# Kernel tuning notes

Hardware: AMD Instinct MI355X
Metric: run time of the kernel (lower is better)

## Reference

```python
import jax, jax.numpy as jnp
import numpy as np

B = 2097152   # ODE-state batch
DIM = 2
HM = 8        # metric hidden
HP = 8        # potential hidden
NV = 2        # number of potential nets
NLV = 1       # hidden layers per potential net


def setup_inputs() -> dict:
    key = jax.random.key(0)
    ks = jax.random.split(key, 16)
    n = lambda k, shp: jax.random.normal(k, shp, dtype=jnp.float32)
    s = 0.5  # weight scale, roughly matching default Linear init magnitude
    return {
        "t": jnp.zeros((1,), jnp.float32),
        "x": n(ks[0], (B, DIM)),
        "mW0": n(ks[1], (HM, DIM)) * s,
        "mb0": n(ks[2], (HM,)) * s,
        "mW1": n(ks[3], (HM, HM)) * s,
        "mb1": n(ks[4], (HM,)) * s,
        "mW2": n(ks[5], (4, HM)) * s,
        "mb2": n(ks[6], (4,)) * s,
        "pW1": n(ks[7], (NV, HP, DIM)) * s,
        "pb1": n(ks[8], (NV, HP)) * s,
        "pW2": n(ks[9], (NV, NLV, HP, HP)) * s,
        "pb2": n(ks[10], (NV, NLV, HP)) * s,
        "pW3": n(ks[11], (NV, 1, HP)) * s,
        "pb3": n(ks[12], (NV, 1)) * s,
    }


def reference(t, x, mW0, mb0, mW1, mb1, mW2, mb2, pW1, pb1, pW2, pb2, pW3, pb3):
    # ---- metric net: Linear->ELU chain, last layer linear, dim -> 4 ----
    h = jax.nn.elu(x @ mW0.T + mb0)
    h = jax.nn.elu(h @ mW1.T + mb1)
    bmat = h @ mW2.T + mb2                      # [B, 4]
    b1, b2, b3, b4 = (bmat[:, 0:1], bmat[:, 1:2], bmat[:, 2:3], bmat[:, 3:4])
    m2 = b1 * b2 + b3 * b4
    mag = jnp.concatenate([b1 ** 2 + b3 ** 2, m2, m2, b2 ** 2 + b4 ** 2], axis=1)  # [B, 4]

    # ---- potential nets, all n_V stacked on leading axis v ----
    f1 = jnp.tanh(jnp.einsum('bi,voi->vbo', x, pW1) + pb1[:, None, :])  # [V, B, HP]
    f2s = []
    f = f1
    for j in range(NLV):  # fixed small loop over structurally distinct layers
        f = jnp.tanh(jnp.einsum('vbp,vqp->vbq', f, pW2[:, j]) + pb2[:, j][:, None, :])
        f2s.append(f)
    f3 = jax.nn.sigmoid(jnp.einsum('vbp,vop->vbo', f, pW3) + pb3[:, None, :])  # [V, B, 1]

    # ---- hand-rolled gradient of potentials (faithful: sigmoid applied to f3 again, as in source) ----
    s = jax.nn.sigmoid(f3)
    grad = (s * (1.0 - s)) * pW3                # [V,B,1]*[V,1,HP] -> [V,B,HP]
    for j in reversed(range(NLV)):
        grad = jnp.einsum('vbq,vqp->vbp', grad * (1.0 - f2s[j] ** 2), pW2[:, j])
    grad = jnp.einsum('vbp,vpi->vbi', grad * (1.0 - f1 ** 2), pW1)  # [V, B, DIM]
    g = jnp.mean(grad, axis=0)                  # sum over n_V then / n_V  -> [B, DIM]

    # ---- combine: out = metric * repeated gradient, row-block sums ----
    g4 = jnp.tile(g, (1, 2))                    # [B, 4]
    out4 = mag * g4
    out = jnp.concatenate([out4[:, :2].sum(1, keepdims=True),
                           out4[:, 2:].sum(1, keepdims=True)], axis=1)  # [B, 2]
    return out
```

## Files before the change

### kernel.cpp

```cpp
#include <hip/hip_runtime.h>

#define NB 2097152
#define HM 8
#define HP 8
#define NV 2

typedef float v2 __attribute__((ext_vector_type(2)));

static __device__ __forceinline__ v2 splat(float s) { return (v2){s, s}; }
static __device__ __forceinline__ v2 vfma(v2 a, v2 b, v2 c) {
    return __builtin_elementwise_fma(a, b, c);
}
static __device__ __forceinline__ v2 vexp2(v2 x) {
    return (v2){__builtin_amdgcn_exp2f(x.x), __builtin_amdgcn_exp2f(x.y)};
}
static __device__ __forceinline__ v2 vclamp9(v2 x) {
    return (v2){__builtin_amdgcn_fmed3f(x.x, -9.f, 9.f),
                __builtin_amdgcn_fmed3f(x.y, -9.f, 9.f)};
}

static __device__ __forceinline__ void tanh8(const v2* z, v2* out) {
    const float a1 = 4.89352455891786e-03f, a3 = 6.37261928875436e-04f,
                a5 = 1.48572235717979e-05f, a7 = 5.12229709037114e-08f,
                a9 = -8.60467152213735e-11f, a11 = 2.00018790482477e-13f,
                a13 = -2.76076847742355e-16f;
    const float b0 = 4.89352518554385e-03f, b2 = 2.26843463243900e-03f,
                b4 = 1.18534705686654e-04f, b6 = 1.19825839466702e-06f;
    v2 p[8], q[8];
#pragma unroll
    for (int i = 0; i < 8; ++i) {
        v2 xc = vclamp9(z[i]);
        v2 t  = xc * xc;
        v2 pp = vfma(t, splat(a13), splat(a11));
        pp = vfma(t, pp, splat(a9));
        pp = vfma(t, pp, splat(a7));
        pp = vfma(t, pp, splat(a5));
        pp = vfma(t, pp, splat(a3));
        pp = vfma(t, pp, splat(a1));
        p[i] = pp * xc;
        v2 qq = vfma(t, splat(b6), splat(b4));
        qq = vfma(t, qq, splat(b2));
        q[i] = vfma(t, qq, splat(b0));
    }
#pragma unroll
    for (int g = 0; g < 2; ++g) {
        const v2* qg = q + g * 4;
        const v2* pg = p + g * 4;
        v2* og = out + g * 4;
        v2 ab = qg[0] * qg[1];
        v2 cd = qg[2] * qg[3];
        v2 abcd = ab * cd;
        v2 inv = (v2){__builtin_amdgcn_rcpf(abcd.x), __builtin_amdgcn_rcpf(abcd.y)};
        v2 s  = cd * inv;
        v2 tt = ab * inv;
        og[0] = pg[0] * (qg[1] * s);
        og[1] = pg[1] * (qg[0] * s);
        og[2] = pg[2] * (qg[3] * tt);
        og[3] = pg[3] * (qg[2] * tt);
    }
}

static __device__ __forceinline__ void elu8(const v2* z, v2* out) {
    const float L2E = 1.4426950408889634f;
#pragma unroll
    for (int i = 0; i < 8; ++i) {
        v2 e  = vexp2(z[i] * splat(L2E));
        v2 em = e - splat(1.f);
        v2 mn = __builtin_elementwise_min(em, splat(0.f));
        out[i] = __builtin_elementwise_max(z[i], mn);
    }
}

static __device__ __forceinline__ v2 vsigmoid(v2 z) {
    const float NL2E = -1.4426950408889634f;
    v2 e = vexp2(z * splat(NL2E));
    e = __builtin_elementwise_min(e, splat(1e18f));
    v2 d = e + splat(1.f);
    float pr  = d.x * d.y;
    float inv = __builtin_amdgcn_rcpf(pr);
    return (v2){inv * d.y, inv * d.x};
}

__global__ __launch_bounds__(256) void odefunc_kernel(
    const float* __restrict__ x,
    const float* __restrict__ mW0, const float* __restrict__ mb0,
    const float* __restrict__ mW1, const float* __restrict__ mb1,
    const float* __restrict__ mW2, const float* __restrict__ mb2,
    const float* __restrict__ pW1, const float* __restrict__ pb1,
    const float* __restrict__ pW2, const float* __restrict__ pb2,
    const float* __restrict__ pW3, const float* __restrict__ pb3,
    float* __restrict__ out)
{
    const int tid = blockIdx.x * blockDim.x + threadIdx.x;
    const int b0  = tid * 2;

    const float4 xv = *reinterpret_cast<const float4*>(x + b0 * 2);
    const v2 x0 = (v2){xv.x, xv.z};
    const v2 x1 = (v2){xv.y, xv.w};
    const v2 one = splat(1.f);

    v2 z[HM], h[HM], h2[HM];
#pragma unroll
    for (int o = 0; o < HM; ++o)
        z[o] = vfma(splat(mW0[o * 2]), x0,
                    vfma(splat(mW0[o * 2 + 1]), x1, splat(mb0[o])));
    elu8(z, h);
#pragma unroll
    for (int o = 0; o < HM; ++o) {
        v2 acc = splat(mb1[o]);
#pragma unroll
        for (int i = 0; i < HM; ++i) acc = vfma(splat(mW1[o * HM + i]), h[i], acc);
        z[o] = acc;
    }
    elu8(z, h2);

    v2 bm[4];
#pragma unroll
    for (int o = 0; o < 4; ++o) {
        v2 acc = splat(mb2[o]);
#pragma unroll
        for (int i = 0; i < HM; ++i) acc = vfma(splat(mW2[o * HM + i]), h2[i], acc);
        bm[o] = acc;
    }
    const v2 m2   = bm[0] * bm[1] + bm[2] * bm[3];
    const v2 mag0 = bm[0] * bm[0] + bm[2] * bm[2];
    const v2 mag3 = bm[1] * bm[1] + bm[3] * bm[3];

    v2 g0 = splat(0.f), g1 = splat(0.f);
#pragma unroll
    for (int v = 0; v < NV; ++v) {
        const float* W1 = pW1 + v * HP * 2;
        const float* B1 = pb1 + v * HP;
        const float* W2 = pW2 + v * HP * HP;
        const float* B2 = pb2 + v * HP;
        const float* W3 = pW3 + v * HP;
        const float  B3 = pb3[v];

        v2 zf[HP], f1[HP], f2[HP];
#pragma unroll
        for (int o = 0; o < HP; ++o)
            zf[o] = vfma(splat(W1[o * 2]), x0,
                         vfma(splat(W1[o * 2 + 1]), x1, splat(B1[o])));
        tanh8(zf, f1);

#pragma unroll
        for (int q = 0; q < HP; ++q) {
            v2 acc = splat(B2[q]);
#pragma unroll
            for (int p = 0; p < HP; ++p) acc = vfma(splat(W2[q * HP + p]), f1[p], acc);
            zf[q] = acc;
        }
        tanh8(zf, f2);

        v2 acc3 = splat(B3);
#pragma unroll
        for (int p = 0; p < HP; ++p) acc3 = vfma(splat(W3[p]), f2[p], acc3);
        const v2 f3 = vsigmoid(acc3);
        const v2 s  = vsigmoid(f3);
        const v2 ss = s * (one - s);

        v2 gq[HP];
#pragma unroll
        for (int q = 0; q < HP; ++q)
            gq[q] = splat(W3[q]) * vfma(-f2[q], f2[q], one);

        v2 gp[HP];
#pragma unroll
        for (int p = 0; p < HP; ++p) {
            v2 acc = splat(0.f);
#pragma unroll
            for (int q = 0; q < HP; ++q) acc = vfma(gq[q], splat(W2[q * HP + p]), acc);
            gp[p] = acc * vfma(-f1[p], f1[p], one);
        }

        v2 gi0 = splat(0.f), gi1 = splat(0.f);
#pragma unroll
        for (int p = 0; p < HP; ++p) {
            gi0 = vfma(gp[p], splat(W1[p * 2]), gi0);
            gi1 = vfma(gp[p], splat(W1[p * 2 + 1]), gi1);
        }
        g0 = vfma(ss, gi0, g0);
        g1 = vfma(ss, gi1, g1);
    }
    g0 = g0 * splat(0.5f);
    g1 = g1 * splat(0.5f);

    const v2 r0 = mag0 * g0 + m2 * g1;
    const v2 r1 = m2 * g0 + mag3 * g1;

    *reinterpret_cast<float4*>(out + b0 * 2) = make_float4(r0.x, r1.x, r0.y, r1.y);
}

extern "C" void kernel_launch(void* const* d_in, const int* in_sizes, int n_in,
                              void* d_out, int out_size, void* d_ws, size_t ws_size,
                              hipStream_t stream) {
    const float* x   = (const float*)d_in[1];
    const float* mW0 = (const float*)d_in[2];
    const float* mb0 = (const float*)d_in[3];
    const float* mW1 = (const float*)d_in[4];
    const float* mb1 = (const float*)d_in[5];
    const float* mW2 = (const float*)d_in[6];
    const float* mb2 = (const float*)d_in[7];
    const float* pW1 = (const float*)d_in[8];
    const float* pb1 = (const float*)d_in[9];
    const float* pW2 = (const float*)d_in[10];
    const float* pb2 = (const float*)d_in[11];
    const float* pW3 = (const float*)d_in[12];
    const float* pb3 = (const float*)d_in[13];
    float* out = (float*)d_out;

    const int threads = 256;
    const int blocks  = NB / (threads * 2);
    odefunc_kernel<<<blocks, threads, 0, stream>>>(
        x, mW0, mb0, mW1, mb1, mW2, mb2, pW1, pb1, pW2, pb2, pW3, pb3, out);
}
```

Measured before the change: 145.4 us.

## Replace rational tanh with exp2-based form and process four rows per thread

The rational polynomial tanh approximation is replaced by tanh = 1 - 2/(exp(2z)+1). It uses one hardware exp2 per element and keeps the shared batched-reciprocal trick, which cuts FMA count in the dominant tanh stages. Each thread now handles two packed pairs (four rows) with half the blocks, which amortises scalar weight loads and index math over more work. The cost is higher register pressure and lower occupancy, plus slightly different tanh accuracy near saturation, where the exp is clamped at 1e8.

```diff
diff --git a/kernel.cpp b/kernel.cpp
--- a/kernel.cpp
+++ b/kernel.cpp
@@ -14,49 +14,30 @@
 static __device__ __forceinline__ v2 vexp2(v2 x) {
     return (v2){__builtin_amdgcn_exp2f(x.x), __builtin_amdgcn_exp2f(x.y)};
 }
-static __device__ __forceinline__ v2 vclamp9(v2 x) {
-    return (v2){__builtin_amdgcn_fmed3f(x.x, -9.f, 9.f),
-                __builtin_amdgcn_fmed3f(x.y, -9.f, 9.f)};
-}
 
 static __device__ __forceinline__ void tanh8(const v2* z, v2* out) {
-    const float a1 = 4.89352455891786e-03f, a3 = 6.37261928875436e-04f,
-                a5 = 1.48572235717979e-05f, a7 = 5.12229709037114e-08f,
-                a9 = -8.60467152213735e-11f, a11 = 2.00018790482477e-13f,
-                a13 = -2.76076847742355e-16f;
-    const float b0 = 4.89352518554385e-03f, b2 = 2.26843463243900e-03f,
-                b4 = 1.18534705686654e-04f, b6 = 1.19825839466702e-06f;
-    v2 p[8], q[8];
+    const float TL2E = 2.8853900817779268f;
+    v2 d[8];
 #pragma unroll
     for (int i = 0; i < 8; ++i) {
-        v2 xc = vclamp9(z[i]);
-        v2 t  = xc * xc;
-        v2 pp = vfma(t, splat(a13), splat(a11));
-        pp = vfma(t, pp, splat(a9));
-        pp = vfma(t, pp, splat(a7));
-        pp = vfma(t, pp, splat(a5));
-        pp = vfma(t, pp, splat(a3));
-        pp = vfma(t, pp, splat(a1));
-        p[i] = pp * xc;
-        v2 qq = vfma(t, splat(b6), splat(b4));
-        qq = vfma(t, qq, splat(b2));
-        q[i] = vfma(t, qq, splat(b0));
+        v2 e = vexp2(z[i] * splat(TL2E));
+        e = __builtin_elementwise_min(e, splat(1e8f));
+        d[i] = e + splat(1.f);
     }
 #pragma unroll
     for (int g = 0; g < 2; ++g) {
-        const v2* qg = q + g * 4;
-        const v2* pg = p + g * 4;
-        v2* og = out + g * 4;
-        v2 ab = qg[0] * qg[1];
-        v2 cd = qg[2] * qg[3];
+        const v2* dg = d + 4 * g;
+        v2* og = out + 4 * g;
+        v2 ab = dg[0] * dg[1];
+        v2 cd = dg[2] * dg[3];
         v2 abcd = ab * cd;
         v2 inv = (v2){__builtin_amdgcn_rcpf(abcd.x), __builtin_amdgcn_rcpf(abcd.y)};
-        v2 s  = cd * inv;
-        v2 tt = ab * inv;
-        og[0] = pg[0] * (qg[1] * s);
-        og[1] = pg[1] * (qg[0] * s);
-        og[2] = pg[2] * (qg[3] * tt);
-        og[3] = pg[3] * (qg[2] * tt);
+        v2 s = cd * inv;
+        v2 t = ab * inv;
+        og[0] = vfma(dg[1] * s, splat(-2.f), splat(1.f));
+        og[1] = vfma(dg[0] * s, splat(-2.f), splat(1.f));
+        og[2] = vfma(dg[3] * t, splat(-2.f), splat(1.f));
+        og[3] = vfma(dg[2] * t, splat(-2.f), splat(1.f));
     }
 }
 
@@ -74,11 +55,113 @@
 static __device__ __forceinline__ v2 vsigmoid(v2 z) {
     const float NL2E = -1.4426950408889634f;
     v2 e = vexp2(z * splat(NL2E));
-    e = __builtin_elementwise_min(e, splat(1e18f));
+    e = __builtin_elementwise_min(e, splat(1e8f));
     v2 d = e + splat(1.f);
     float pr  = d.x * d.y;
     float inv = __builtin_amdgcn_rcpf(pr);
     return (v2){inv * d.y, inv * d.x};
+}
+
+static __device__ __forceinline__ void compute_pair(
+    v2 x0, v2 x1,
+    const float* __restrict__ mW0, const float* __restrict__ mb0,
+    const float* __restrict__ mW1, const float* __restrict__ mb1,
+    const float* __restrict__ mW2, const float* __restrict__ mb2,
+    const float* __restrict__ pW1, const float* __restrict__ pb1,
+    const float* __restrict__ pW2, const float* __restrict__ pb2,
+    const float* __restrict__ pW3, const float* __restrict__ pb3,
+    v2& r0, v2& r1)
+{
+    const v2 one = splat(1.f);
+
+    v2 z[HM], h[HM], h2[HM];
+#pragma unroll
+    for (int o = 0; o < HM; ++o)
+        z[o] = vfma(splat(mW0[o * 2]), x0,
+                    vfma(splat(mW0[o * 2 + 1]), x1, splat(mb0[o])));
+    elu8(z, h);
+#pragma unroll
+    for (int o = 0; o < HM; ++o) {
+        v2 acc = splat(mb1[o]);
+#pragma unroll
+        for (int i = 0; i < HM; ++i) acc = vfma(splat(mW1[o * HM + i]), h[i], acc);
+        z[o] = acc;
+    }
+    elu8(z, h2);
+
+    v2 bm[4];
+#pragma unroll
+    for (int o = 0; o < 4; ++o) {
+        v2 acc = splat(mb2[o]);
+#pragma unroll
+        for (int i = 0; i < HM; ++i) acc = vfma(splat(mW2[o * HM + i]), h2[i], acc);
+        bm[o] = acc;
+    }
+    const v2 m2   = bm[0] * bm[1] + bm[2] * bm[3];
+    const v2 mag0 = bm[0] * bm[0] + bm[2] * bm[2];
+    const v2 mag3 = bm[1] * bm[1] + bm[3] * bm[3];
+
+    v2 g0 = splat(0.f), g1 = splat(0.f);
+#pragma unroll
+    for (int v = 0; v < NV; ++v) {
+        const float* W1 = pW1 + v * HP * 2;
+        const float* B1 = pb1 + v * HP;
+        const float* W2 = pW2 + v * HP * HP;
+        const float* B2 = pb2 + v * HP;
+        const float* W3 = pW3 + v * HP;
+        const float  B3 = pb3[v];
+
+        v2 zf[HP], f1[HP], f2[HP];
+#pragma unroll
+        for (int o = 0; o < HP; ++o)
+            zf[o] = vfma(splat(W1[o * 2]), x0,
+                         vfma(splat(W1[o * 2 + 1]), x1, splat(B1[o])));
+        tanh8(zf, f1);
+
+#pragma unroll
+        for (int q = 0; q < HP; ++q) {
+            v2 acc = splat(B2[q]);
+#pragma unroll
+            for (int p = 0; p < HP; ++p) acc = vfma(splat(W2[q * HP + p]), f1[p], acc);
+            zf[q] = acc;
+        }
+        tanh8(zf, f2);
+
+        v2 acc3 = splat(B3);
+#pragma unroll
+        for (int p = 0; p < HP; ++p) acc3 = vfma(splat(W3[p]), f2[p], acc3);
+        const v2 f3 = vsigmoid(acc3);
+        const v2 s  = vsigmoid(f3);
+        const v2 ss = s * (one - s);
+
+        v2 gq[HP];
+#pragma unroll
+        for (int q = 0; q < HP; ++q)
+            gq[q] = splat(W3[q]) * vfma(-f2[q], f2[q], one);
+
+        v2 gp[HP];
+#pragma unroll
+        for (int p = 0; p < HP; ++p) {
+            v2 acc = splat(0.f);
+#pragma unroll
+            for (int q = 0; q < HP; ++q) acc = vfma(gq[q], splat(W2[q * HP + p]), acc);
+            gp[p] = acc * vfma(-f1[p], f1[p], one);
+        }
+
+        v2 gi0 = splat(0.f), gi1 = splat(0.f);
+#pragma unroll
+        for (int p = 0; p < HP; ++p) {
+            gi0 = vfma(gp[p], splat(W1[p * 2]), gi0);
+            gi1 = vfma(gp[p], splat(W1[p * 2 + 1]), gi1);
+        }
+        g0 = vfma(ss, gi0, g0);
+        g1 = vfma(ss, gi1, g1);
+    }
+    g0 = g0 * splat(0.5f);
+    g1 = g1 * splat(0.5f);
+
+    r0 = mag0 * g0 + m2 * g1;
+    r1 = m2 * g0 + mag3 * g1;
 }
 
 __global__ __launch_bounds__(256) void odefunc_kernel(
@@ -92,103 +175,21 @@
     float* __restrict__ out)
 {
     const int tid = blockIdx.x * blockDim.x + threadIdx.x;
-    const int b0  = tid * 2;
-
-    const float4 xv = *reinterpret_cast<const float4*>(x + b0 * 2);
-    const v2 x0 = (v2){xv.x, xv.z};
-    const v2 x1 = (v2){xv.y, xv.w};
-    const v2 one = splat(1.f);
-
-    v2 z[HM], h[HM], h2[HM];
-#pragma unroll
-    for (int o = 0; o < HM; ++o)
-        z[o] = vfma(splat(mW0[o * 2]), x0,
-                    vfma(splat(mW0[o * 2 + 1]), x1, splat(mb0[o])));
-    elu8(z, h);
-#pragma unroll
-    for (int o = 0; o < HM; ++o) {
-        v2 acc = splat(mb1[o]);
-#pragma unroll
-        for (int i = 0; i < HM; ++i) acc = vfma(splat(mW1[o * HM + i]), h[i], acc);
-        z[o] = acc;
-    }
-    elu8(z, h2);
-
-    v2 bm[4];
-#pragma unroll
-    for (int o = 0; o < 4; ++o) {
-        v2 acc = splat(mb2[o]);
-#pragma unroll
-        for (int i = 0; i < HM; ++i) acc = vfma(splat(mW2[o * HM + i]), h2[i], acc);
-        bm[o] = acc;
-    }
-    const v2 m2   = bm[0] * bm[1] + bm[2] * bm[3];
-    const v2 mag0 = bm[0] * bm[0] + bm[2] * bm[2];
-    const v2 mag3 = bm[1] * bm[1] + bm[3] * bm[3];
-
-    v2 g0 = splat(0.f), g1 = splat(0.f);
-#pragma unroll
-    for (int v = 0; v < NV; ++v) {
-        const float* W1 = pW1 + v * HP * 2;
-        const float* B1 = pb1 + v * HP;
-        const float* W2 = pW2 + v * HP * HP;
-        const float* B2 = pb2 + v * HP;
-        const float* W3 = pW3 + v * HP;
-        const float  B3 = pb3[v];
-
-        v2 zf[HP], f1[HP], f2[HP];
-#pragma unroll
-        for (int o = 0; o < HP; ++o)
-            zf[o] = vfma(splat(W1[o * 2]), x0,
-                         vfma(splat(W1[o * 2 + 1]), x1, splat(B1[o])));
-        tanh8(zf, f1);
-
-#pragma unroll
-        for (int q = 0; q < HP; ++q) {
-            v2 acc = splat(B2[q]);
-#pragma unroll
-            for (int p = 0; p < HP; ++p) acc = vfma(splat(W2[q * HP + p]), f1[p], acc);
-            zf[q] = acc;
-        }
-        tanh8(zf, f2);
-
-        v2 acc3 = splat(B3);
-#pragma unroll
-        for (int p = 0; p < HP; ++p) acc3 = vfma(splat(W3[p]), f2[p], acc3);
-        const v2 f3 = vsigmoid(acc3);
-        const v2 s  = vsigmoid(f3);
-        const v2 ss = s * (one - s);
-
-        v2 gq[HP];
-#pragma unroll
-        for (int q = 0; q < HP; ++q)
-            gq[q] = splat(W3[q]) * vfma(-f2[q], f2[q], one);
-
-        v2 gp[HP];
-#pragma unroll
-        for (int p = 0; p < HP; ++p) {
-            v2 acc = splat(0.f);
-#pragma unroll
-            for (int q = 0; q < HP; ++q) acc = vfma(gq[q], splat(W2[q * HP + p]), acc);
-            gp[p] = acc * vfma(-f1[p], f1[p], one);
-        }
-
-        v2 gi0 = splat(0.f), gi1 = splat(0.f);
-#pragma unroll
-        for (int p = 0; p < HP; ++p) {
-            gi0 = vfma(gp[p], splat(W1[p * 2]), gi0);
-            gi1 = vfma(gp[p], splat(W1[p * 2 + 1]), gi1);
-        }
-        g0 = vfma(ss, gi0, g0);
-        g1 = vfma(ss, gi1, g1);
-    }
-    g0 = g0 * splat(0.5f);
-    g1 = g1 * splat(0.5f);
-
-    const v2 r0 = mag0 * g0 + m2 * g1;
-    const v2 r1 = m2 * g0 + mag3 * g1;
-
-    *reinterpret_cast<float4*>(out + b0 * 2) = make_float4(r0.x, r1.x, r0.y, r1.y);
+    const int b0  = tid * 4;
+
+    const float4 xvA = *reinterpret_cast<const float4*>(x + b0 * 2);
+    const float4 xvB = *reinterpret_cast<const float4*>(x + b0 * 2 + 4);
+
+    v2 r0A, r1A, r0B, r1B;
+    compute_pair((v2){xvA.x, xvA.z}, (v2){xvA.y, xvA.w},
+                 mW0, mb0, mW1, mb1, mW2, mb2,
+                 pW1, pb1, pW2, pb2, pW3, pb3, r0A, r1A);
+    compute_pair((v2){xvB.x, xvB.z}, (v2){xvB.y, xvB.w},
+                 mW0, mb0, mW1, mb1, mW2, mb2,
+                 pW1, pb1, pW2, pb2, pW3, pb3, r0B, r1B);
+
+    *reinterpret_cast<float4*>(out + b0 * 2)     = make_float4(r0A.x, r1A.x, r0A.y, r1A.y);
+    *reinterpret_cast<float4*>(out + b0 * 2 + 4) = make_float4(r0B.x, r1B.x, r0B.y, r1B.y);
 }
 
 extern "C" void kernel_launch(void* const* d_in, const int* in_sizes, int n_in,
@@ -210,7 +211,7 @@
     float* out = (float*)d_out;
 
     const int threads = 256;
-    const int blocks  = NB / (threads * 2);
+    const int blocks  = NB / (threads * 4);
     odefunc_kernel<<<blocks, threads, 0, stream>>>(
         x, mW0, mb0, mW1, mb1, mW2, mb2, pW1, pb1, pW2, pb2, pW3, pb3, out);
 }
```

Measured after the change: 144.0 us. About the same (-1.0%).
